# Kernel tuning notes

Hardware: AMD Instinct MI355X
Metric: run time of the kernel (lower is better)

The kernel has to match this reference:

```python
import jax, jax.numpy as jnp
import numpy as np

N_NODES = 100000
N_EDGES = 1250000
IN_CH = 128
OUT_CH = 64


def setup_inputs() -> dict:
    key = jax.random.key(0)
    k1, k2, k3, k4 = jax.random.split(key, 4)
    x = jax.random.normal(k1, (N_NODES, IN_CH), dtype=jnp.float32)
    edge_index = jax.random.randint(k2, (2, N_EDGES), 0, N_NODES, dtype=jnp.int64)
    edge_weight = jax.random.uniform(k3, (N_EDGES,), dtype=jnp.float32)
    # Xavier-uniform weight, zero bias (as in reset_parameters)
    limit = float(np.sqrt(6.0 / (IN_CH + OUT_CH)))
    W = jax.random.uniform(k4, (IN_CH, OUT_CH), dtype=jnp.float32, minval=-limit, maxval=limit)
    b = jnp.zeros((OUT_CH,), dtype=jnp.float32)
    return {"x": x, "edge_index": edge_index, "edge_weight": edge_weight, "W": W, "b": b}


def reference(x, edge_index, edge_weight, W, b):
    # Dense transform: [N, in] @ [in, out] -> [N, out]
    h = jnp.matmul(x, W)
    row, col = edge_index[0], edge_index[1]
    n = h.shape[0]
    # Weighted in-degree via scatter-add on destination (row)
    deg = jnp.zeros((n,), dtype=h.dtype).at[row].add(edge_weight)
    # deg^-0.5 with inf (deg==0) replaced by 0
    deg_inv_sqrt = jnp.where(deg == 0, jnp.zeros_like(deg), deg ** -0.5)
    norm = deg_inv_sqrt[row] * deg_inv_sqrt[col]  # [E]
    # Gather source features, normalize, scatter-add to destinations
    out = jnp.zeros_like(h).at[row].add(h[col] * norm[:, None])
    return out + b
```

## Files before the change

### kernel.cpp

```cpp
#include <hip/hip_runtime.h>

#define N_NODES 100000
#define N_EDGES 1250000
#define IN_CH 128
#define OUT_CH 64

#define NPB 128
#define ACCS2 33
#define NBINS 782
#define LSTRIDE 783
#define RECCAP 2048
#define NB1 384
#define B1T 512
#define CH1 ((N_EDGES + NB1 - 1) / NB1)
#define MAXU ((CH1 + B1T - 1) / B1T)
#define NG4 ((NBINS + 3) / 4)
#define GEMM_BLOCKS ((N_NODES + 127) / 128)

#define QSCALE 8192.0f
#define QBIAS_F 8388608.0f
#define QBIAS_U 8388608u
#define INV_QSCALE 1.220703125e-4f
#define SCALE_DEG 33554432.0f
#define INV_SCALE_DEG 2.9802322387695312e-08f

typedef __attribute__((ext_vector_type(8))) short short8;
typedef __attribute__((ext_vector_type(4))) float f32x4;

__device__ inline unsigned int f2bf(float f) {
    unsigned int u = __float_as_uint(f);
    unsigned int r = ((u >> 16) & 1u) + 0x7FFFu;
    return (u + r) >> 16;
}
__device__ inline float bf_lo(unsigned int p) { return __uint_as_float(p << 16); }
__device__ inline float bf_hi(unsigned int p) { return __uint_as_float(p & 0xFFFF0000u); }

__device__ inline unsigned long long qpacks(unsigned int p, float sc) {
    unsigned int lo = (unsigned int)__float2int_rn(fmaf(bf_lo(p), sc, QBIAS_F));
    unsigned int hi = (unsigned int)__float2int_rn(fmaf(bf_hi(p), sc, QBIAS_F));
    return ((unsigned long long)hi << 32) | (unsigned long long)lo;
}

__global__ __launch_bounds__(B1T) void sort_kernel(const int* __restrict__ ei,
                                                   const float* __restrict__ ew,
                                                   const float* __restrict__ W,
                                                   unsigned int* __restrict__ Wb,
                                                   int* __restrict__ lscan2d,
                                                   int2* __restrict__ brec) {
    __shared__ int2 srec[CH1];
    __shared__ int shist[NBINS];
    __shared__ int sscan[NBINS + 2];
    __shared__ int ssum[256];
    const int tid = threadIdx.x;

    if (blockIdx.x >= NB1) {
        int g = (blockIdx.x - NB1) * B1T + tid;
        if (g < 1024) {
            int c = g >> 8;
            int t4 = (g >> 6) & 3;
            int l = g & 63;
            int q = l >> 4, r15 = l & 15;
            unsigned int o[4];
#pragma unroll
            for (int jj = 0; jj < 4; ++jj) {
                float f0 = W[(c * 32 + q * 8 + 2 * jj)     * OUT_CH + t4 * 16 + r15];
                float f1 = W[(c * 32 + q * 8 + 2 * jj + 1) * OUT_CH + t4 * 16 + r15];
                o[jj] = f2bf(f0) | (f2bf(f1) << 16);
            }
            *(uint4*)(Wb + (size_t)g * 4) = make_uint4(o[0], o[1], o[2], o[3]);
        }
        return;
    }

    for (int i = tid; i < NBINS; i += B1T) shist[i] = 0;
    __syncthreads();

    const int e0 = blockIdx.x * CH1;
    const int total = (e0 + CH1 < N_EDGES) ? CH1 : N_EDGES - e0;

    int rowv[MAXU], colv[MAXU];
    float wv[MAXU];
#pragma unroll
    for (int u = 0; u < MAXU; ++u) {
        int e = e0 + tid + u * B1T;
        bool ok = (tid + u * B1T) < total;
        rowv[u] = ok ? ei[e] : -1;
        colv[u] = ok ? ei[N_EDGES + e] : 0;
        wv[u]   = ok ? ew[e] : 0.0f;
        if (ok) atomicAdd(&shist[rowv[u] >> 7], 1);
    }
    __syncthreads();

    int a0 = 0, a1 = 0, a2 = 0, a3 = 0, part = 0;
    const int b0 = tid * 4;
    if (tid < 256) {
        a0 = (b0 + 0 < NBINS) ? shist[b0 + 0] : 0;
        a1 = (b0 + 1 < NBINS) ? shist[b0 + 1] : 0;
        a2 = (b0 + 2 < NBINS) ? shist[b0 + 2] : 0;
        a3 = (b0 + 3 < NBINS) ? shist[b0 + 3] : 0;
        part = a0 + a1 + a2 + a3;
        ssum[tid] = part;
    }
    __syncthreads();
#pragma unroll
    for (int d = 1; d < 256; d <<= 1) {
        int add = 0;
        if (tid >= d && tid < 256) add = ssum[tid - d];
        __syncthreads();
        if (tid < 256) ssum[tid] += add;
        __syncthreads();
    }
    if (tid < 256) {
        int base = ssum[tid] - part;
        if (b0 + 0 <= NBINS) sscan[b0 + 0] = base;
        if (b0 + 1 <= NBINS) sscan[b0 + 1] = base + a0;
        if (b0 + 2 <= NBINS) sscan[b0 + 2] = base + a0 + a1;
        if (b0 + 3 <= NBINS) sscan[b0 + 3] = base + a0 + a1 + a2;
    }
    __syncthreads();

    for (int i = tid; i < NBINS; i += B1T) shist[i] = 0;
    __syncthreads();

#pragma unroll
    for (int u = 0; u < MAXU; ++u) {
        if (rowv[u] >= 0) {
            int bb = rowv[u] >> 7;
            int rk = atomicAdd(&shist[bb], 1);
            srec[sscan[bb] + rk] = make_int2(((rowv[u] & 127) << 17) | colv[u],
                                             __float_as_int(wv[u]));
        }
    }
    __syncthreads();

    for (int i = tid; i < total; i += B1T) brec[e0 + i] = srec[i];
    int* lrow = lscan2d + blockIdx.x * LSTRIDE;
    for (int i = tid; i <= NBINS; i += B1T) lrow[i] = sscan[i];
}

__global__ __launch_bounds__(512) void prep_gemm_kernel(const float* __restrict__ x,
                                                        const unsigned int* __restrict__ Wb,
                                                        const int* __restrict__ lscan2d,
                                                        const int2* __restrict__ brec,
                                                        int* __restrict__ brec2,
                                                        float* __restrict__ dis,
                                                        int* __restrict__ qcnt,
                                                        int* __restrict__ mtot,
                                                        unsigned int* __restrict__ hs) {
    const int tid = threadIdx.x;

    if (blockIdx.x < NG4) {
        __shared__ int lsc[NB1][6];
        __shared__ int soff[NB1];
        __shared__ int recs[RECCAP];
        __shared__ unsigned long long degcnt[512];
        const int b0bin = blockIdx.x * 4;

        degcnt[tid] = 0ull;
        if (tid < NB1) {
            const int* lrow = lscan2d + tid * LSTRIDE;
#pragma unroll
            for (int j = 0; j < 5; ++j) {
                int bi = b0bin + j;
                lsc[tid][j] = lrow[(bi < NBINS) ? bi : NBINS];
            }
        }
        __syncthreads();

        for (int j = 0; j < 4; ++j) {
            int bin = b0bin + j;
            if (bin >= NBINS) break;
            if (tid < NB1) soff[tid] = lsc[tid][j + 1] - lsc[tid][j];
            __syncthreads();
#pragma unroll
            for (int d = 1; d < NB1; d <<= 1) {
                int add = 0;
                if (tid >= d && tid < NB1) add = soff[tid - d];
                __syncthreads();
                if (tid < NB1) soff[tid] += add;
                __syncthreads();
            }
            const int m = soff[NB1 - 1];
            const int mc = (m < RECCAP) ? m : RECCAP;

            for (int p = tid; p < m; p += 512) {
                int lo = 0, hi = NB1 - 1;
                while (lo < hi) {
                    int mid = (lo + hi) >> 1;
                    if (soff[mid] > p) hi = mid; else lo = mid + 1;
                }
                int excl = (lo == 0) ? 0 : soff[lo - 1];
                int2 r = brec[(size_t)lo * CH1 + lsc[lo][j] + (p - excl)];
                if (p < RECCAP) recs[p] = r.x;
                unsigned int qd =
                    (unsigned int)__float2int_rn(__int_as_float(r.y) * SCALE_DEG);
                atomicAdd(&degcnt[j * NPB + (r.x >> 17)],
                          (1ull << 32) | (unsigned long long)qd);
            }
            __syncthreads();

            for (int p = tid; p < mc; p += 512)
                brec2[(size_t)bin * RECCAP + p] = recs[p];
            if (tid == 0) mtot[bin] = mc;
            __syncthreads();
        }

        int node = b0bin * NPB + tid;
        if ((b0bin + (tid >> 7)) < NBINS && node < N_NODES) {
            unsigned long long dc = degcnt[tid];
            float d = (float)(unsigned int)dc * INV_SCALE_DEG;
            dis[node]  = (d == 0.0f) ? 0.0f : (1.0f / sqrtf(d));
            qcnt[node] = (int)(dc >> 32);
        }
    } else {
        const int blk  = blockIdx.x - NG4;
        const int w    = tid >> 6;
        const int lane = tid & 63;
        const int q    = lane >> 4, r15 = lane & 15;
        const int node = blk * 128 + w * 16 + r15;
        const int nl   = (node < N_NODES) ? node : N_NODES - 1;
        const float* xrow = x + (size_t)nl * IN_CH;

        f32x4 acc[4];
#pragma unroll
        for (int t = 0; t < 4; ++t) acc[t] = (f32x4){0.f, 0.f, 0.f, 0.f};

#pragma unroll
        for (int c = 0; c < 4; ++c) {
            float4 xa = *(const float4*)(xrow + c * 32 + q * 8);
            float4 xb = *(const float4*)(xrow + c * 32 + q * 8 + 4);
            short8 bfrag;
            bfrag[0] = (short)f2bf(xa.x); bfrag[1] = (short)f2bf(xa.y);
            bfrag[2] = (short)f2bf(xa.z); bfrag[3] = (short)f2bf(xa.w);
            bfrag[4] = (short)f2bf(xb.x); bfrag[5] = (short)f2bf(xb.y);
            bfrag[6] = (short)f2bf(xb.z); bfrag[7] = (short)f2bf(xb.w);
#pragma unroll
            for (int t = 0; t < 4; ++t) {
                short8 afrag = *(const short8*)(Wb + (size_t)((c * 4 + t) * 64 + lane) * 4);
                acc[t] = __builtin_amdgcn_mfma_f32_16x16x32_bf16(afrag, bfrag, acc[t], 0, 0, 0);
            }
        }

        if (node < N_NODES) {
#pragma unroll
            for (int t = 0; t < 4; ++t) {
                unsigned int p0 = f2bf(acc[t][0]) | (f2bf(acc[t][1]) << 16);
                unsigned int p1 = f2bf(acc[t][2]) | (f2bf(acc[t][3]) << 16);
                *(uint2*)(hs + (size_t)node * 32 + t * 8 + q * 2) = make_uint2(p0, p1);
            }
        }
    }
}

__global__ __launch_bounds__(512) void gather_kernel(const int* __restrict__ mtot,
                                                     const int* __restrict__ brec2,
                                                     const uint4* __restrict__ hs,
                                                     const float* __restrict__ dis,
                                                     const int* __restrict__ qcnt,
                                                     const float* __restrict__ b,
                                                     float* __restrict__ out) {
    __shared__ unsigned long long acc[NPB * ACCS2];
    const int tid = threadIdx.x;
    const int blk = blockIdx.x;
    for (int k = tid; k < NPB * ACCS2; k += 512) acc[k] = 0ull;
    __syncthreads();

    const int m = mtot[blk];
    const int rbase = blk * RECCAP;

    const int wid = tid >> 6, lane = tid & 63;
    const int sub = lane >> 3, l8 = lane & 7;

    for (int j0 = wid * 32; j0 < m; j0 += 256) {
        bool ok[4];
        int rec[4];
        uint4 p[4];
        float sc[4];
#pragma unroll
        for (int s = 0; s < 4; ++s) {
            int jj = j0 + 8 * s + sub;
            ok[s] = jj < m;
            rec[s] = ok[s] ? brec2[rbase + jj] : 0;
        }
#pragma unroll
        for (int s = 0; s < 4; ++s) {
            p[s] = ok[s] ? hs[(size_t)(rec[s] & 0x1FFFF) * 8 + l8]
                         : make_uint4(0, 0, 0, 0);
            sc[s] = ok[s] ? QSCALE * dis[rec[s] & 0x1FFFF] : 0.0f;
        }
#pragma unroll
        for (int s = 0; s < 4; ++s) {
            if (ok[s]) {
                int ba = (rec[s] >> 17) * ACCS2 + 4 * l8;
                atomicAdd(&acc[ba + 0], qpacks(p[s].x, sc[s]));
                atomicAdd(&acc[ba + 1], qpacks(p[s].y, sc[s]));
                atomicAdd(&acc[ba + 2], qpacks(p[s].z, sc[s]));
                atomicAdd(&acc[ba + 3], qpacks(p[s].w, sc[s]));
            }
        }
    }
    __syncthreads();

    const unsigned int* acc32 = (const unsigned int*)acc;
    float bc = b[lane];
    int half = lane & 1, slot = lane >> 1;
#pragma unroll 4
    for (int r = 0; r < 16; ++r) {
        int nl = wid * 16 + r;
        int node = blk * NPB + nl;
        if (node < N_NODES) {
            unsigned int raw = acc32[(nl * ACCS2 + slot) * 2 + half];
            int qsum = (int)(raw - (unsigned int)qcnt[node] * QBIAS_U);
            float di = dis[node] * INV_QSCALE;
            out[(size_t)node * OUT_CH + lane] = (float)qsum * di + bc;
        }
    }
}

extern "C" void kernel_launch(void* const* d_in, const int* in_sizes, int n_in,
                              void* d_out, int out_size, void* d_ws, size_t ws_size,
                              hipStream_t stream) {
    const float* x  = (const float*)d_in[0];
    const int*   ei = (const int*)d_in[1];
    const float* ew = (const float*)d_in[2];
    const float* W  = (const float*)d_in[3];
    const float* b  = (const float*)d_in[4];
    float* out = (float*)d_out;

    unsigned int* hs = (unsigned int*)d_ws;
    unsigned int* Wb = hs + (size_t)N_NODES * 32;
    int* lscan2d = (int*)(Wb + 4096);
    int* mtot    = lscan2d + (size_t)NB1 * LSTRIDE;
    float* dis   = (float*)(mtot + 800);
    int* qcnt    = (int*)(dis + N_NODES);
    int* brec2   = qcnt + N_NODES;
    int2* brec   = (int2*)(brec2 + (size_t)NBINS * RECCAP);
    (void)ws_size; (void)in_sizes; (void)n_in; (void)out_size;

    sort_kernel<<<NB1 + 2, B1T, 0, stream>>>(ei, ew, W, Wb, lscan2d, brec);
    prep_gemm_kernel<<<NG4 + GEMM_BLOCKS, 512, 0, stream>>>(x, Wb, lscan2d, brec,
                                                            brec2, dis, qcnt,
                                                            mtot, hs);
    gather_kernel<<<NBINS, 512, 0, stream>>>(mtot, brec2, (const uint4*)hs,
                                             dis, qcnt, b, out);
}
```

Baseline: 161.1 us.

## Sort bin records by row and accumulate runs in registers before atomics

The prep kernel now counting-sorts each bin's edge records by destination row in shared memory, so the gather kernel sees each row's edges contiguously. The gather kernel gives each 8-lane group a contiguous slice of records, accumulates same-row contributions in float registers, and issues one packed quantized LDS atomic per row run instead of one per edge. The bias-count correction is tracked per block in shared memory, so the global qcnt array goes away. This cuts LDS atomic traffic but adds a sort pass with extra barriers and can leave slices unbalanced when rows are skewed.

New measurement: 166.9 us. 1.04x slower.

```diff
diff --git a/kernel.cpp b/kernel.cpp
--- a/kernel.cpp
+++ b/kernel.cpp
@@ -35,9 +35,9 @@
 __device__ inline float bf_lo(unsigned int p) { return __uint_as_float(p << 16); }
 __device__ inline float bf_hi(unsigned int p) { return __uint_as_float(p & 0xFFFF0000u); }
 
-__device__ inline unsigned long long qpacks(unsigned int p, float sc) {
-    unsigned int lo = (unsigned int)__float2int_rn(fmaf(bf_lo(p), sc, QBIAS_F));
-    unsigned int hi = (unsigned int)__float2int_rn(fmaf(bf_hi(p), sc, QBIAS_F));
+__device__ inline unsigned long long fpack(float c0, float c1) {
+    unsigned int lo = (unsigned int)__float2int_rn(fmaf(c0, QSCALE, QBIAS_F));
+    unsigned int hi = (unsigned int)__float2int_rn(fmaf(c1, QSCALE, QBIAS_F));
     return ((unsigned long long)hi << 32) | (unsigned long long)lo;
 }
 
@@ -144,7 +144,6 @@
                                                         const int2* __restrict__ brec,
                                                         int* __restrict__ brec2,
                                                         float* __restrict__ dis,
-                                                        int* __restrict__ qcnt,
                                                         int* __restrict__ mtot,
                                                         unsigned int* __restrict__ hs) {
     const int tid = threadIdx.x;
@@ -153,6 +152,9 @@
         __shared__ int lsc[NB1][6];
         __shared__ int soff[NB1];
         __shared__ int recs[RECCAP];
+        __shared__ int recs2[RECCAP];
+        __shared__ int rowbase[NPB];
+        __shared__ int rnk[NPB];
         __shared__ unsigned long long degcnt[512];
         const int b0bin = blockIdx.x * 4;
 
@@ -199,8 +201,35 @@
             }
             __syncthreads();
 
+            if (tid < 64) {
+                int c0 = (int)(degcnt[j * NPB + 2 * tid] >> 32);
+                int c1 = (int)(degcnt[j * NPB + 2 * tid + 1] >> 32);
+                int s = c0 + c1;
+#pragma unroll
+                for (int d = 1; d < 64; d <<= 1) {
+                    int t2 = __shfl_up(s, d);
+                    if (tid >= d) s += t2;
+                }
+                int eb = s - c0 - c1;
+                rowbase[2 * tid]     = eb;
+                rowbase[2 * tid + 1] = eb + c0;
+                rnk[2 * tid] = 0; rnk[2 * tid + 1] = 0;
+            }
+            __syncthreads();
+            if (m > RECCAP) {
+                for (int p = tid; p < RECCAP; p += 512) recs2[p] = 0;
+                __syncthreads();
+            }
+            for (int p = tid; p < mc; p += 512) {
+                int r = recs[p];
+                int row = r >> 17;
+                int slot = rowbase[row] + atomicAdd(&rnk[row], 1);
+                if (slot < RECCAP) recs2[slot] = r;
+            }
+            __syncthreads();
+
             for (int p = tid; p < mc; p += 512)
-                brec2[(size_t)bin * RECCAP + p] = recs[p];
+                brec2[(size_t)bin * RECCAP + p] = recs2[p];
             if (tid == 0) mtot[bin] = mc;
             __syncthreads();
         }
@@ -209,8 +238,7 @@
         if ((b0bin + (tid >> 7)) < NBINS && node < N_NODES) {
             unsigned long long dc = degcnt[tid];
             float d = (float)(unsigned int)dc * INV_SCALE_DEG;
-            dis[node]  = (d == 0.0f) ? 0.0f : (1.0f / sqrtf(d));
-            qcnt[node] = (int)(dc >> 32);
+            dis[node] = (d == 0.0f) ? 0.0f : (1.0f / sqrtf(d));
         }
     } else {
         const int blk  = blockIdx.x - NG4;
@@ -256,52 +284,86 @@
                                                      const int* __restrict__ brec2,
                                                      const uint4* __restrict__ hs,
                                                      const float* __restrict__ dis,
-                                                     const int* __restrict__ qcnt,
                                                      const float* __restrict__ b,
                                                      float* __restrict__ out) {
     __shared__ unsigned long long acc[NPB * ACCS2];
+    __shared__ int cnt[NPB];
     const int tid = threadIdx.x;
     const int blk = blockIdx.x;
     for (int k = tid; k < NPB * ACCS2; k += 512) acc[k] = 0ull;
+    if (tid < NPB) cnt[tid] = 0;
     __syncthreads();
 
     const int m = mtot[blk];
     const int rbase = blk * RECCAP;
-
-    const int wid = tid >> 6, lane = tid & 63;
-    const int sub = lane >> 3, l8 = lane & 7;
-
-    for (int j0 = wid * 32; j0 < m; j0 += 256) {
+    const int grp = tid >> 3, l8 = tid & 7;
+    const int per = (m + 63) >> 6;
+    const int p0 = grp * per;
+    const int p1 = (p0 + per < m) ? p0 + per : m;
+
+    float a[8];
+#pragma unroll
+    for (int jj = 0; jj < 8; ++jj) a[jj] = 0.0f;
+    int currow = -1;
+
+    for (int p = p0; p < p1; p += 4) {
         bool ok[4];
         int rec[4];
-        uint4 p[4];
+        uint4 h[4];
         float sc[4];
 #pragma unroll
         for (int s = 0; s < 4; ++s) {
-            int jj = j0 + 8 * s + sub;
-            ok[s] = jj < m;
-            rec[s] = ok[s] ? brec2[rbase + jj] : 0;
+            int pp = p + s;
+            ok[s] = pp < p1;
+            rec[s] = ok[s] ? brec2[rbase + pp] : 0;
         }
 #pragma unroll
         for (int s = 0; s < 4; ++s) {
-            p[s] = ok[s] ? hs[(size_t)(rec[s] & 0x1FFFF) * 8 + l8]
-                         : make_uint4(0, 0, 0, 0);
-            sc[s] = ok[s] ? QSCALE * dis[rec[s] & 0x1FFFF] : 0.0f;
+            int col = rec[s] & 0x1FFFF;
+            h[s]  = ok[s] ? hs[(size_t)col * 8 + l8] : make_uint4(0, 0, 0, 0);
+            sc[s] = ok[s] ? dis[col] : 0.0f;
         }
 #pragma unroll
         for (int s = 0; s < 4; ++s) {
             if (ok[s]) {
-                int ba = (rec[s] >> 17) * ACCS2 + 4 * l8;
-                atomicAdd(&acc[ba + 0], qpacks(p[s].x, sc[s]));
-                atomicAdd(&acc[ba + 1], qpacks(p[s].y, sc[s]));
-                atomicAdd(&acc[ba + 2], qpacks(p[s].z, sc[s]));
-                atomicAdd(&acc[ba + 3], qpacks(p[s].w, sc[s]));
-            }
-        }
+                int row = rec[s] >> 17;
+                if (row != currow) {
+                    if (currow >= 0) {
+                        int ba = currow * ACCS2 + 4 * l8;
+                        atomicAdd(&acc[ba + 0], fpack(a[0], a[1]));
+                        atomicAdd(&acc[ba + 1], fpack(a[2], a[3]));
+                        atomicAdd(&acc[ba + 2], fpack(a[4], a[5]));
+                        atomicAdd(&acc[ba + 3], fpack(a[6], a[7]));
+                        if (l8 == 0) atomicAdd(&cnt[currow], 1);
+                    }
+#pragma unroll
+                    for (int jj = 0; jj < 8; ++jj) a[jj] = 0.0f;
+                    currow = row;
+                }
+                float s0 = sc[s];
+                a[0] = fmaf(bf_lo(h[s].x), s0, a[0]);
+                a[1] = fmaf(bf_hi(h[s].x), s0, a[1]);
+                a[2] = fmaf(bf_lo(h[s].y), s0, a[2]);
+                a[3] = fmaf(bf_hi(h[s].y), s0, a[3]);
+                a[4] = fmaf(bf_lo(h[s].z), s0, a[4]);
+                a[5] = fmaf(bf_hi(h[s].z), s0, a[5]);
+                a[6] = fmaf(bf_lo(h[s].w), s0, a[6]);
+                a[7] = fmaf(bf_hi(h[s].w), s0, a[7]);
+            }
+        }
+    }
+    if (currow >= 0) {
+        int ba = currow * ACCS2 + 4 * l8;
+        atomicAdd(&acc[ba + 0], fpack(a[0], a[1]));
+        atomicAdd(&acc[ba + 1], fpack(a[2], a[3]));
+        atomicAdd(&acc[ba + 2], fpack(a[4], a[5]));
+        atomicAdd(&acc[ba + 3], fpack(a[6], a[7]));
+        if (l8 == 0) atomicAdd(&cnt[currow], 1);
     }
     __syncthreads();
 
     const unsigned int* acc32 = (const unsigned int*)acc;
+    const int wid = tid >> 6, lane = tid & 63;
     float bc = b[lane];
     int half = lane & 1, slot = lane >> 1;
 #pragma unroll 4
@@ -310,7 +372,7 @@
         int node = blk * NPB + nl;
         if (node < N_NODES) {
             unsigned int raw = acc32[(nl * ACCS2 + slot) * 2 + half];
-            int qsum = (int)(raw - (unsigned int)qcnt[node] * QBIAS_U);
+            int qsum = (int)(raw - (unsigned int)cnt[nl] * QBIAS_U);
             float di = dis[node] * INV_QSCALE;
             out[(size_t)node * OUT_CH + lane] = (float)qsum * di + bc;
         }
@@ -332,15 +394,13 @@
     int* lscan2d = (int*)(Wb + 4096);
     int* mtot    = lscan2d + (size_t)NB1 * LSTRIDE;
     float* dis   = (float*)(mtot + 800);
-    int* qcnt    = (int*)(dis + N_NODES);
-    int* brec2   = qcnt + N_NODES;
+    int* brec2   = (int*)(dis + N_NODES);
     int2* brec   = (int2*)(brec2 + (size_t)NBINS * RECCAP);
     (void)ws_size; (void)in_sizes; (void)n_in; (void)out_size;
 
     sort_kernel<<<NB1 + 2, B1T, 0, stream>>>(ei, ew, W, Wb, lscan2d, brec);
     prep_gemm_kernel<<<NG4 + GEMM_BLOCKS, 512, 0, stream>>>(x, Wb, lscan2d, brec,
-                                                            brec2, dis, qcnt,
-                                                            mtot, hs);
+                                                            brec2, dis, mtot, hs);
     gather_kernel<<<NBINS, 512, 0, stream>>>(mtot, brec2, (const uint4*)hs,
-                                             dis, qcnt, b, out);
-}
+                                             dis, b, out);
+}
```

## Use wave-shuffle scans and split gather bins across two half-blocks

Applied to the files above, without the earlier changes.

Replaces the shared-memory Hillis-Steele prefix scans in the sort and prep kernels with wavefront shuffle scans plus a small per-wave sum combine, cutting many __syncthreads barriers. The gather kernel now launches two 256-thread blocks per bin, each owning 64 destination rows with half the LDS accumulator, to raise occupancy and parallelism. Each half-block still reads every record of the bin and discards the ones for the other half, so record loads are duplicated.

Result: slower. 171.3 us (+6.3%).

```diff
diff --git a/kernel.cpp b/kernel.cpp
--- a/kernel.cpp
+++ b/kernel.cpp
@@ -50,7 +50,7 @@
     __shared__ int2 srec[CH1];
     __shared__ int shist[NBINS];
     __shared__ int sscan[NBINS + 2];
-    __shared__ int ssum[256];
+    __shared__ int swsum[8];
     const int tid = threadIdx.x;
 
     if (blockIdx.x >= NB1) {
@@ -91,6 +91,7 @@
     }
     __syncthreads();
 
+    const int lanev = tid & 63, wvid = tid >> 6;
     int a0 = 0, a1 = 0, a2 = 0, a3 = 0, part = 0;
     const int b0 = tid * 4;
     if (tid < 256) {
@@ -99,19 +100,20 @@
         a2 = (b0 + 2 < NBINS) ? shist[b0 + 2] : 0;
         a3 = (b0 + 3 < NBINS) ? shist[b0 + 3] : 0;
         part = a0 + a1 + a2 + a3;
-        ssum[tid] = part;
-    }
-    __syncthreads();
-#pragma unroll
-    for (int d = 1; d < 256; d <<= 1) {
-        int add = 0;
-        if (tid >= d && tid < 256) add = ssum[tid - d];
-        __syncthreads();
-        if (tid < 256) ssum[tid] += add;
-        __syncthreads();
-    }
+    }
+    int s = part;
+#pragma unroll
+    for (int d = 1; d < 64; d <<= 1) {
+        int t2 = __shfl_up(s, d);
+        if (lanev >= d) s += t2;
+    }
+    if (tid < 256 && lanev == 63) swsum[wvid] = s;
+    __syncthreads();
     if (tid < 256) {
-        int base = ssum[tid] - part;
+        int wbase = 0;
+#pragma unroll
+        for (int k = 0; k < 4; ++k) if (k < wvid) wbase += swsum[k];
+        int base = wbase + s - part;
         if (b0 + 0 <= NBINS) sscan[b0 + 0] = base;
         if (b0 + 1 <= NBINS) sscan[b0 + 1] = base + a0;
         if (b0 + 2 <= NBINS) sscan[b0 + 2] = base + a0 + a1;
@@ -153,8 +155,10 @@
         __shared__ int lsc[NB1][6];
         __shared__ int soff[NB1];
         __shared__ int recs[RECCAP];
+        __shared__ int swsum[8];
         __shared__ unsigned long long degcnt[512];
         const int b0bin = blockIdx.x * 4;
+        const int lanev = tid & 63, wvid = tid >> 6;
 
         degcnt[tid] = 0ull;
         if (tid < NB1) {
@@ -170,17 +174,26 @@
         for (int j = 0; j < 4; ++j) {
             int bin = b0bin + j;
             if (bin >= NBINS) break;
-            if (tid < NB1) soff[tid] = lsc[tid][j + 1] - lsc[tid][j];
+
+            int len = (tid < NB1) ? (lsc[tid][j + 1] - lsc[tid][j]) : 0;
+            int s = len;
+#pragma unroll
+            for (int d = 1; d < 64; d <<= 1) {
+                int t2 = __shfl_up(s, d);
+                if (lanev >= d) s += t2;
+            }
+            if (lanev == 63) swsum[wvid] = s;
             __syncthreads();
-#pragma unroll
-            for (int d = 1; d < NB1; d <<= 1) {
-                int add = 0;
-                if (tid >= d && tid < NB1) add = soff[tid - d];
-                __syncthreads();
-                if (tid < NB1) soff[tid] += add;
-                __syncthreads();
-            }
-            const int m = soff[NB1 - 1];
+            int wbase = 0, m = 0;
+#pragma unroll
+            for (int k = 0; k < 8; ++k) {
+                int v = swsum[k];
+                if (k < wvid) wbase += v;
+                m += v;
+            }
+            if (tid < NB1) soff[tid] = wbase + s;
+            __syncthreads();
+
             const int mc = (m < RECCAP) ? m : RECCAP;
 
             for (int p = tid; p < m; p += 512) {
@@ -252,64 +265,65 @@
     }
 }
 
-__global__ __launch_bounds__(512) void gather_kernel(const int* __restrict__ mtot,
+__global__ __launch_bounds__(256) void gather_kernel(const int* __restrict__ mtot,
                                                      const int* __restrict__ brec2,
                                                      const uint4* __restrict__ hs,
                                                      const float* __restrict__ dis,
                                                      const int* __restrict__ qcnt,
                                                      const float* __restrict__ b,
                                                      float* __restrict__ out) {
-    __shared__ unsigned long long acc[NPB * ACCS2];
-    const int tid = threadIdx.x;
-    const int blk = blockIdx.x;
-    for (int k = tid; k < NPB * ACCS2; k += 512) acc[k] = 0ull;
+    __shared__ unsigned long long acc[64 * ACCS2];
+    const int tid  = threadIdx.x;
+    const int blk  = blockIdx.x >> 1;
+    const int half = blockIdx.x & 1;
+    for (int k = tid; k < 64 * ACCS2; k += 256) acc[k] = 0ull;
     __syncthreads();
 
     const int m = mtot[blk];
     const int rbase = blk * RECCAP;
-
-    const int wid = tid >> 6, lane = tid & 63;
-    const int sub = lane >> 3, l8 = lane & 7;
-
-    for (int j0 = wid * 32; j0 < m; j0 += 256) {
+    const int grp = tid >> 3, l8 = tid & 7;
+
+    for (int p0 = grp * 4; p0 < m; p0 += 128) {
         bool ok[4];
         int rec[4];
-        uint4 p[4];
+        uint4 h[4];
         float sc[4];
 #pragma unroll
         for (int s = 0; s < 4; ++s) {
-            int jj = j0 + 8 * s + sub;
-            ok[s] = jj < m;
-            rec[s] = ok[s] ? brec2[rbase + jj] : 0;
+            int pp = p0 + s;
+            int r = (pp < m) ? brec2[rbase + pp] : 0;
+            rec[s] = r;
+            ok[s] = (pp < m) && (((r >> 23) & 1) == half);
         }
 #pragma unroll
         for (int s = 0; s < 4; ++s) {
-            p[s] = ok[s] ? hs[(size_t)(rec[s] & 0x1FFFF) * 8 + l8]
-                         : make_uint4(0, 0, 0, 0);
-            sc[s] = ok[s] ? QSCALE * dis[rec[s] & 0x1FFFF] : 0.0f;
+            int col = rec[s] & 0x1FFFF;
+            h[s]  = ok[s] ? hs[(size_t)col * 8 + l8] : make_uint4(0, 0, 0, 0);
+            sc[s] = ok[s] ? QSCALE * dis[col] : 0.0f;
         }
 #pragma unroll
         for (int s = 0; s < 4; ++s) {
             if (ok[s]) {
-                int ba = (rec[s] >> 17) * ACCS2 + 4 * l8;
-                atomicAdd(&acc[ba + 0], qpacks(p[s].x, sc[s]));
-                atomicAdd(&acc[ba + 1], qpacks(p[s].y, sc[s]));
-                atomicAdd(&acc[ba + 2], qpacks(p[s].z, sc[s]));
-                atomicAdd(&acc[ba + 3], qpacks(p[s].w, sc[s]));
+                int ba = ((rec[s] >> 17) & 63) * ACCS2 + 4 * l8;
+                atomicAdd(&acc[ba + 0], qpacks(h[s].x, sc[s]));
+                atomicAdd(&acc[ba + 1], qpacks(h[s].y, sc[s]));
+                atomicAdd(&acc[ba + 2], qpacks(h[s].z, sc[s]));
+                atomicAdd(&acc[ba + 3], qpacks(h[s].w, sc[s]));
             }
         }
     }
     __syncthreads();
 
     const unsigned int* acc32 = (const unsigned int*)acc;
+    const int wid = tid >> 6, lane = tid & 63;
     float bc = b[lane];
-    int half = lane & 1, slot = lane >> 1;
+    int chalf = lane & 1, slot = lane >> 1;
 #pragma unroll 4
     for (int r = 0; r < 16; ++r) {
-        int nl = wid * 16 + r;
-        int node = blk * NPB + nl;
+        int rl = wid * 16 + r;
+        int node = blk * NPB + half * 64 + rl;
         if (node < N_NODES) {
-            unsigned int raw = acc32[(nl * ACCS2 + slot) * 2 + half];
+            unsigned int raw = acc32[(rl * ACCS2 + slot) * 2 + chalf];
             int qsum = (int)(raw - (unsigned int)qcnt[node] * QBIAS_U);
             float di = dis[node] * INV_QSCALE;
             out[(size_t)node * OUT_CH + lane] = (float)qsum * di + bc;
@@ -341,6 +355,6 @@
     prep_gemm_kernel<<<NG4 + GEMM_BLOCKS, 512, 0, stream>>>(x, Wb, lscan2d, brec,
                                                             brec2, dis, qcnt,
                                                             mtot, hs);
-    gather_kernel<<<NBINS, 512, 0, stream>>>(mtot, brec2, (const uint4*)hs,
-                                             dis, qcnt, b, out);
-}
+    gather_kernel<<<NBINS * 2, 256, 0, stream>>>(mtot, brec2, (const uint4*)hs,
+                                                 dis, qcnt, b, out);
+}
```
